# Kernel tuning notes

Measured on AMD Instinct MI355X. Metric: run time of the kernel, lower is better.

## Reference

```python
import jax, jax.numpy as jnp
import numpy as np

B, BARS, BEATS, FRAC = 64, 16, 4, 8
IN_F = 10 * 47 * 2  # 940
LIN_OUT = 100
BEAT_H = 16
BAR_H = 32


def _p(key, shape, scale=0.05):
    return jax.random.normal(key, shape, dtype=jnp.float32) * scale


def setup_inputs() -> dict:
    key = jax.random.key(0)
    ks = jax.random.split(key, 16)
    return {
        "channels": jax.random.normal(ks[0], (B, BARS, BEATS, FRAC, 10, 2, 47), dtype=jnp.float32),
        "lin_w": _p(ks[1], (LIN_OUT, IN_F)),
        "lin_b": _p(ks[2], (LIN_OUT,)),
        # beats LSTM (unidirectional), PyTorch gate order i,f,g,o
        "b_wih": _p(ks[3], (4 * BEAT_H, LIN_OUT)),
        "b_whh": _p(ks[4], (4 * BEAT_H, BEAT_H)),
        "b_bih": _p(ks[5], (4 * BEAT_H,)),
        "b_bhh": _p(ks[6], (4 * BEAT_H,)),
        # bars LSTM, bidirectional: forward (f_) and reverse (r_) directions
        "f_wih": _p(ks[7], (4 * BAR_H, BEAT_H)),
        "f_whh": _p(ks[8], (4 * BAR_H, BAR_H)),
        "f_bih": _p(ks[9], (4 * BAR_H,)),
        "f_bhh": _p(ks[10], (4 * BAR_H,)),
        "r_wih": _p(ks[11], (4 * BAR_H, BEAT_H)),
        "r_whh": _p(ks[12], (4 * BAR_H, BAR_H)),
        "r_bih": _p(ks[13], (4 * BAR_H,)),
        "r_bhh": _p(ks[14], (4 * BAR_H,)),
    }


def lstm(x, wih, whh, bih, bhh):
    """PyTorch-semantics LSTM, batch_first. x: [N, T, F] -> h_seq [N, T, H]."""
    N = x.shape[0]
    H = whh.shape[1]
    # precompute input contribution for all timesteps
    xg = jnp.einsum('ntf,gf->ntg', x, wih) + (bih + bhh)  # [N, T, 4H]

    def step(carry, xt):
        h, c = carry
        gates = xt + h @ whh.T  # [N, 4H]
        i, f, g, o = jnp.split(gates, 4, axis=-1)
        c = jax.nn.sigmoid(f) * c + jax.nn.sigmoid(i) * jnp.tanh(g)
        h = jax.nn.sigmoid(o) * jnp.tanh(c)
        return (h, c), h

    h0 = jnp.zeros((N, H), x.dtype)
    _, hs = jax.lax.scan(step, (h0, h0), jnp.swapaxes(xg, 0, 1))  # [T, N, H]
    return jnp.swapaxes(hs, 0, 1)


def bilstm(x, f_wih, f_whh, f_bih, f_bhh, r_wih, r_whh, r_bih, r_bhh):
    fwd = lstm(x, f_wih, f_whh, f_bih, f_bhh)
    bwd = jnp.flip(lstm(jnp.flip(x, axis=1), r_wih, r_whh, r_bih, r_bhh), axis=1)
    return jnp.concatenate([fwd, bwd], axis=-1)


def reference(channels, lin_w, lin_b,
              b_wih, b_whh, b_bih, b_bhh,
              f_wih, f_whh, f_bih, f_bhh,
              r_wih, r_whh, r_bih, r_bhh):
    # channels: [B, bars, beats, frac, 10, 2, 47]
    x = jnp.swapaxes(channels, -1, -2)  # [..., 10, 47, 2]
    x = x.reshape(*x.shape[:4], IN_F)   # squash dims 4..6 -> 940
    x = jax.nn.relu(x @ lin_w.T + lin_b)  # [B, bars, beats, frac, 100]

    # Distributed depth=2: fold (B, bars, beats) into batch, seq over frac
    xb = x.reshape(B * BARS * BEATS, FRAC, LIN_OUT)
    beats = lstm(xb, b_wih, b_whh, b_bih, b_bhh)
    beats = beats.reshape(B, BARS, BEATS, FRAC, BEAT_H)

    # last fraction hidden state, then Distributed depth=1 over beats axis
    xl = beats[:, :, :, -1].reshape(B * BARS, BEATS, BEAT_H)
    bars = bilstm(xl, f_wih, f_whh, f_bih, f_bhh, r_wih, r_whh, r_bih, r_bhh)
    bars = bars.reshape(B, BARS, BEATS, 2 * BAR_H)
    return beats, bars
```

## Files before the change

### kernel.cpp

```cpp
#include <hip/hip_runtime.h>
#include <hip/hip_bf16.h>

typedef float f32x4 __attribute__((ext_vector_type(4)));
typedef short bf16x8 __attribute__((ext_vector_type(8)));
typedef short bf16x4 __attribute__((ext_vector_type(4)));

#define MFMA16(a, b, c) __builtin_amdgcn_mfma_f32_16x16x32_bf16(a, b, c, 0, 0, 0)

constexpr int K1  = 940;
constexpr int KP2 = 1024;
constexpr int NP  = 112;
constexpr int OSL = 136;

__device__ __forceinline__ float sigf(float x) { return 1.f / (1.f + __expf(-x)); }
__device__ __forceinline__ float tanhfast(float x) { return 2.f / (1.f + __expf(-2.f * x)) - 1.f; }

__device__ __forceinline__ short f2b(float x) {
  __hip_bfloat16 b = __float2bfloat16(x);
  return *reinterpret_cast<short*>(&b);
}

__device__ __forceinline__ void lds_barrier() {
  asm volatile("s_waitcnt lgkmcnt(0)" ::: "memory");
  __builtin_amdgcn_s_barrier();
  __builtin_amdgcn_sched_barrier(0);
}

__global__ void prep_kernel(const float* __restrict__ lin_w,
                            const float* __restrict__ b_wih,
                            __hip_bfloat16* __restrict__ w2,
                            __hip_bfloat16* __restrict__ bw2) {
  int idx = blockIdx.x * 256 + threadIdx.x;
  if (idx < NP * KP2) {
    int n = idx >> 10, k = idx & 1023;
    float v = 0.f;
    if (n < 100 && k < K1) {
      int c10 = k / 94, rem = k - c10 * 94;
      int c2 = rem / 47, c47 = rem - c2 * 47;
      int f = c10 * 94 + c47 * 2 + c2;
      v = lin_w[n * K1 + f];
    }
    w2[idx] = __float2bfloat16(v);
  } else {
    int i2 = idx - NP * KP2;
    if (i2 < 64 * 128) {
      int g = i2 >> 7, k = i2 & 127;
      bw2[i2] = __float2bfloat16((k < 100) ? b_wih[g * 100 + k] : 0.f);
    }
  }
}

__global__ __launch_bounds__(256, 2)
void fused_encoder(const float* __restrict__ ch,
                   const __hip_bfloat16* __restrict__ w2,
                   const float* __restrict__ lin_b,
                   const __hip_bfloat16* __restrict__ bw2,
                   const float* __restrict__ bih,
                   const float* __restrict__ bhh,
                   const float* __restrict__ whh,
                   const float* __restrict__ fwih, const float* __restrict__ fwhh,
                   const float* __restrict__ fbih, const float* __restrict__ fbhh,
                   const float* __restrict__ rwih, const float* __restrict__ rwhh,
                   const float* __restrict__ rbih, const float* __restrict__ rbhh,
                   float* __restrict__ beats,
                   float* __restrict__ bars) {
  __shared__ __align__(16) char smem[45056];
  char* As = smem;
  char* Bw = smem + 16384;
  __hip_bfloat16* out_s = reinterpret_cast<__hip_bfloat16*>(smem);
  float*          xg_s  = reinterpret_cast<float*>(smem + 17408);
  float (*hlast)[16]    = reinterpret_cast<float(*)[16]>(smem + 34048);
  float (*hb)[32]       = reinterpret_cast<float(*)[32]>(smem + 34560);
  float (*gact)[128]    = reinterpret_cast<float(*)[128]>(smem + 34816);

  const int tid = threadIdx.x;
  const int w = tid >> 6, lane = tid & 63;
  const int l16 = lane & 15, bq = lane >> 4;

  float lb[7];
#pragma unroll
  for (int nt = 0; nt < 7; ++nt) {
    int col = nt * 16 + l16;
    lb[nt] = (col < 100) ? lin_b[col] : 0.f;
  }

  f32x4 acc[7] = {};
  float4 rA[8];
  bf16x8 bst[8];

  const float4 f40{0.f, 0.f, 0.f, 0.f};

  const int acolf = (lane & 31) * 4;
  const float* asrc = ch + (long)(blockIdx.x * 64 + w * 16 + (lane >> 5)) * K1 + acolf;
  auto ldA = [&](int c) {
    const float* p = asrc + c * 128;
    if (c < 7) {
#pragma unroll
      for (int j = 0; j < 8; ++j)
        rA[j] = *reinterpret_cast<const float4*>(p + (long)j * 2 * K1);
    } else {
      const bool ok = acolf < 44;
#pragma unroll
      for (int j = 0; j < 8; ++j)
        rA[j] = ok ? *reinterpret_cast<const float4*>(p + (long)j * 2 * K1) : f40;
    }
  };
  auto stA = [&]() {
#pragma unroll
    for (int j = 0; j < 8; ++j) {
      const int row = w * 16 + (lane >> 5) + 2 * j;
      const int byte = row * 256 + (((lane & 31) * 8) ^ ((row & 7) << 4));
      bf16x4 v = {f2b(rA[j].x), f2b(rA[j].y), f2b(rA[j].z), f2b(rA[j].w)};
      *reinterpret_cast<bf16x4*>(As + byte) = v;
    }
  };

  const int sn = tid >> 1;
  const int khb = (tid & 1) * 128;
  auto ldB = [&](int c) {
    if (sn < NP) {
      const __hip_bfloat16* src = w2 + sn * KP2 + c * 128 + (tid & 1) * 64;
#pragma unroll
      for (int j = 0; j < 8; ++j)
        bst[j] = *reinterpret_cast<const bf16x8*>(src + j * 8);
    }
  };
  auto stB = [&]() {
    if (sn < NP) {
      const int swz = (sn & 7) << 4;
#pragma unroll
      for (int j = 0; j < 8; ++j)
        *reinterpret_cast<bf16x8*>(Bw + sn * 256 + ((khb + j * 16) ^ swz)) = bst[j];
    }
  };

  ldA(0);
  ldB(0);

  const int fsw = (l16 & 7) << 4;
  const int abase = (w * 16 + l16) * 256;

#pragma unroll
  for (int c = 0; c < 8; ++c) {
    stA();
    stB();
    lds_barrier();
    if (c < 7) { ldA(c + 1); ldB(c + 1); }
#pragma unroll
    for (int ks = 0; ks < 4; ++ks) {
      const int ko = (ks * 64 + bq * 16);
      bf16x8 a = *reinterpret_cast<const bf16x8*>(As + abase + (ko ^ fsw));
#pragma unroll
      for (int nt = 0; nt < 7; ++nt) {
        bf16x8 b = *reinterpret_cast<const bf16x8*>(
            Bw + (nt * 16 + l16) * 256 + (ko ^ fsw));
        acc[nt] = MFMA16(a, b, acc[nt]);
      }
    }
    lds_barrier();
  }

#pragma unroll
  for (int nt = 0; nt < 7; ++nt) {
    const int col = nt * 16 + l16;
#pragma unroll
    for (int r = 0; r < 4; ++r) {
      float v = fmaxf(acc[nt][r] + lb[nt], 0.f);
      out_s[(w * 16 + bq * 4 + r) * OSL + col] = __float2bfloat16((col < 100) ? v : 0.f);
    }
  }
#pragma unroll
  for (int r = 0; r < 4; ++r)
    out_s[(w * 16 + bq * 4 + r) * OSL + 112 + l16] = __float2bfloat16(0.f);

  {
    bf16x8 av[4];
#pragma unroll
    for (int s = 0; s < 4; ++s)
      av[s] = *reinterpret_cast<const bf16x8*>(&out_s[(w * 16 + l16) * OSL + s * 32 + bq * 8]);
    f32x4 xacc[4] = {};
#pragma unroll
    for (int gt = 0; gt < 4; ++gt) {
#pragma unroll
      for (int s = 0; s < 4; ++s) {
        bf16x8 b = *reinterpret_cast<const bf16x8*>(&bw2[(gt * 16 + l16) * 128 + s * 32 + bq * 8]);
        xacc[gt] = MFMA16(av[s], b, xacc[gt]);
      }
    }
#pragma unroll
    for (int gt = 0; gt < 4; ++gt) {
      const int gate = gt * 16 + l16;
      const float bias = bih[gate] + bhh[gate];
#pragma unroll
      for (int r = 0; r < 4; ++r)
        xg_s[(w * 16 + bq * 4 + r) * 65 + gate] = xacc[gt][r] + bias;
    }
  }

  {
    const int cell = lane & 15;
    float wr[16];
#pragma unroll
    for (int u = 0; u < 16; ++u) wr[u] = whh[lane * 16 + u];
    float xv0[8], xv1[8];
#pragma unroll
    for (int t = 0; t < 8; ++t) {
      xv0[t] = xg_s[(w * 16 + t) * 65 + lane];
      xv1[t] = xg_s[(w * 16 + 8 + t) * 65 + lane];
    }
    float h0[16], h1[16];
#pragma unroll
    for (int u = 0; u < 16; ++u) { h0[u] = 0.f; h1[u] = 0.f; }
    float c0 = 0.f, c1 = 0.f;
    const long sg0 = (long)blockIdx.x * 8 + 2 * w;
    const long sg1 = sg0 + 1;
#pragma unroll
    for (int t = 0; t < 8; ++t) {
      float p0 = xv0[t], p1 = xv1[t];
#pragma unroll
      for (int u = 0; u < 16; ++u) { p0 += wr[u] * h0[u]; p1 += wr[u] * h1[u]; }
      const bool istanh = (lane >= 32 && lane < 48);
      float a0 = istanh ? tanhfast(p0) : sigf(p0);
      float a1 = istanh ? tanhfast(p1) : sigf(p1);
      float gi0 = __shfl(a0, cell),      gi1 = __shfl(a1, cell);
      float gf0 = __shfl(a0, cell + 16), gf1 = __shfl(a1, cell + 16);
      float gg0 = __shfl(a0, cell + 32), gg1 = __shfl(a1, cell + 32);
      float go0 = __shfl(a0, cell + 48), go1 = __shfl(a1, cell + 48);
      c0 = gf0 * c0 + gi0 * gg0;
      c1 = gf1 * c1 + gi1 * gg1;
      float hn0 = go0 * tanhfast(c0);
      float hn1 = go1 * tanhfast(c1);
#pragma unroll
      for (int u = 0; u < 16; ++u) { h0[u] = __shfl(hn0, u); h1[u] = __shfl(hn1, u); }
      if (lane < 16) {
        beats[sg0 * 128 + t * 16 + lane] = hn0;
        beats[sg1 * 128 + t * 16 + lane] = hn1;
        if (t == 7) {
          hlast[2 * w][lane]     = hn0;
          hlast[2 * w + 1][lane] = hn1;
        }
      }
    }
  }
  __syncthreads();

  {
    const int dir = tid >> 7, g = tid & 127;
    const float* wihp = dir ? rwih : fwih;
    const float* whhp = dir ? rwhh : fwhh;
    const float bias = dir ? (rbih[g] + rbhh[g]) : (fbih[g] + fbhh[g]);
    float wi[16], wh[32];
#pragma unroll
    for (int u = 0; u < 16; ++u) wi[u] = wihp[g * 16 + u];
#pragma unroll
    for (int u = 0; u < 32; ++u) wh[u] = whhp[g * 32 + u];
    for (int b2 = 0; b2 < 2; ++b2) {
      const int n = blockIdx.x * 2 + b2;
      float c = 0.f;
      if (g < 32) hb[dir][g] = 0.f;
      __syncthreads();
      for (int t = 0; t < 4; ++t) {
        const int tt = dir ? (3 - t) : t;
        float pre = bias;
#pragma unroll
        for (int u = 0; u < 16; ++u) pre += wi[u] * hlast[b2 * 4 + tt][u];
#pragma unroll
        for (int u = 0; u < 32; ++u) pre += wh[u] * hb[dir][u];
        gact[dir][g] = (g >= 64 && g < 96) ? tanhfast(pre) : sigf(pre);
        __syncthreads();
        if (g < 32) {
          c = gact[dir][32 + g] * c + gact[dir][g] * gact[dir][64 + g];
          float hn = gact[dir][96 + g] * tanhfast(c);
          hb[dir][g] = hn;
          bars[(n * 4 + tt) * 64 + dir * 32 + g] = hn;
        }
        __syncthreads();
      }
    }
  }
}

extern "C" void kernel_launch(void* const* d_in, const int* in_sizes, int n_in,
                              void* d_out, int out_size, void* d_ws, size_t ws_size,
                              hipStream_t stream) {
  const float* ch    = (const float*)d_in[0];
  const float* lin_w = (const float*)d_in[1];
  const float* lin_b = (const float*)d_in[2];
  const float* b_wih = (const float*)d_in[3];
  const float* b_whh = (const float*)d_in[4];
  const float* b_bih = (const float*)d_in[5];
  const float* b_bhh = (const float*)d_in[6];
  const float* f_wih = (const float*)d_in[7];
  const float* f_whh = (const float*)d_in[8];
  const float* f_bih = (const float*)d_in[9];
  const float* f_bhh = (const float*)d_in[10];
  const float* r_wih = (const float*)d_in[11];
  const float* r_whh = (const float*)d_in[12];
  const float* r_bih = (const float*)d_in[13];
  const float* r_bhh = (const float*)d_in[14];

  char* ws = (char*)d_ws;
  __hip_bfloat16* w2  = (__hip_bfloat16*)ws;
  __hip_bfloat16* bw2 = (__hip_bfloat16*)(ws + 229376);
  float*          out = (float*)d_out;

  prep_kernel<<<480, 256, 0, stream>>>(lin_w, b_wih, w2, bw2);
  fused_encoder<<<512, 256, 0, stream>>>(ch, w2, lin_b, bw2, b_bih, b_bhh,
                                         b_whh,
                                         f_wih, f_whh, f_bih, f_bhh,
                                         r_wih, r_whh, r_bih, r_bhh,
                                         out, out + 524288);
}
```

Measured before the change: 231.4 us.

## Split fused encoder into DMA-pipelined GEMM and separate LSTM kernel

The fused encoder is split into two kernels: a linear GEMM that writes bf16 activations to a workspace, and an LSTM kernel that reads them back. The GEMM now streams the weight matrix straight into LDS with global_load_lds. It uses double-buffered B tiles stored pre-swizzled in chunks by the prep kernel, and it overlaps the next chunk's loads with the current MFMAs. This aims to cut register staging and per-chunk barriers in the GEMM, and lets the LSTM kernel run with its own resource limits. In exchange it adds an extra launch and a global round trip for the intermediate activations.

Measured after the change: 234.1 us. No clear change (+1.2%).

```diff
diff --git a/kernel.cpp b/kernel.cpp
--- a/kernel.cpp
+++ b/kernel.cpp
@@ -8,9 +8,10 @@
 #define MFMA16(a, b, c) __builtin_amdgcn_mfma_f32_16x16x32_bf16(a, b, c, 0, 0, 0)
 
 constexpr int K1  = 940;
-constexpr int KP2 = 1024;
 constexpr int NP  = 112;
 constexpr int OSL = 136;
+constexpr int CHE = 14336;
+constexpr int CHB = 28672;
 
 __device__ __forceinline__ float sigf(float x) { return 1.f / (1.f + __expf(-x)); }
 __device__ __forceinline__ float tanhfast(float x) { return 2.f / (1.f + __expf(-2.f * x)) - 1.f; }
@@ -20,18 +21,18 @@
   return *reinterpret_cast<short*>(&b);
 }
 
-__device__ __forceinline__ void lds_barrier() {
-  asm volatile("s_waitcnt lgkmcnt(0)" ::: "memory");
-  __builtin_amdgcn_s_barrier();
-  __builtin_amdgcn_sched_barrier(0);
+__device__ __forceinline__ void gl_lds16(const void* g, void* l) {
+  __builtin_amdgcn_global_load_lds(
+      (const __attribute__((address_space(1))) unsigned int*)g,
+      (__attribute__((address_space(3))) unsigned int*)l, 16, 0, 0);
 }
 
 __global__ void prep_kernel(const float* __restrict__ lin_w,
                             const float* __restrict__ b_wih,
-                            __hip_bfloat16* __restrict__ w2,
+                            __hip_bfloat16* __restrict__ w2c,
                             __hip_bfloat16* __restrict__ bw2) {
   int idx = blockIdx.x * 256 + threadIdx.x;
-  if (idx < NP * KP2) {
+  if (idx < NP * 1024) {
     int n = idx >> 10, k = idx & 1023;
     float v = 0.f;
     if (n < 100 && k < K1) {
@@ -40,9 +41,10 @@
       int f = c10 * 94 + c47 * 2 + c2;
       v = lin_w[n * K1 + f];
     }
-    w2[idx] = __float2bfloat16(v);
+    int c = k >> 7, kk = k & 127;
+    w2c[c * CHE + n * 128 + (kk ^ ((n & 7) << 3))] = __float2bfloat16(v);
   } else {
-    int i2 = idx - NP * KP2;
+    int i2 = idx - NP * 1024;
     if (i2 < 64 * 128) {
       int g = i2 >> 7, k = i2 & 127;
       bw2[i2] = __float2bfloat16((k < 100) ? b_wih[g * 100 + k] : 0.f);
@@ -51,47 +53,23 @@
 }
 
 __global__ __launch_bounds__(256, 2)
-void fused_encoder(const float* __restrict__ ch,
-                   const __hip_bfloat16* __restrict__ w2,
-                   const float* __restrict__ lin_b,
-                   const __hip_bfloat16* __restrict__ bw2,
-                   const float* __restrict__ bih,
-                   const float* __restrict__ bhh,
-                   const float* __restrict__ whh,
-                   const float* __restrict__ fwih, const float* __restrict__ fwhh,
-                   const float* __restrict__ fbih, const float* __restrict__ fbhh,
-                   const float* __restrict__ rwih, const float* __restrict__ rwhh,
-                   const float* __restrict__ rbih, const float* __restrict__ rbhh,
-                   float* __restrict__ beats,
-                   float* __restrict__ bars) {
-  __shared__ __align__(16) char smem[45056];
+void linear_gemm(const float* __restrict__ ch,
+                 const __hip_bfloat16* __restrict__ w2c,
+                 const float* __restrict__ lin_b,
+                 __hip_bfloat16* __restrict__ out1) {
+  __shared__ __align__(16) char smem[73728];
   char* As = smem;
-  char* Bw = smem + 16384;
-  __hip_bfloat16* out_s = reinterpret_cast<__hip_bfloat16*>(smem);
-  float*          xg_s  = reinterpret_cast<float*>(smem + 17408);
-  float (*hlast)[16]    = reinterpret_cast<float(*)[16]>(smem + 34048);
-  float (*hb)[32]       = reinterpret_cast<float(*)[32]>(smem + 34560);
-  float (*gact)[128]    = reinterpret_cast<float(*)[128]>(smem + 34816);
+  char* Bs = smem + 16384;
 
   const int tid = threadIdx.x;
   const int w = tid >> 6, lane = tid & 63;
   const int l16 = lane & 15, bq = lane >> 4;
-
-  float lb[7];
-#pragma unroll
-  for (int nt = 0; nt < 7; ++nt) {
-    int col = nt * 16 + l16;
-    lb[nt] = (col < 100) ? lin_b[col] : 0.f;
-  }
-
-  f32x4 acc[7] = {};
+  const int row0 = blockIdx.x * 64 + w * 16;
+
   float4 rA[8];
-  bf16x8 bst[8];
-
   const float4 f40{0.f, 0.f, 0.f, 0.f};
-
   const int acolf = (lane & 31) * 4;
-  const float* asrc = ch + (long)(blockIdx.x * 64 + w * 16 + (lane >> 5)) * K1 + acolf;
+  const float* asrc = ch + (long)(row0 + (lane >> 5)) * K1 + acolf;
   auto ldA = [&](int c) {
     const float* p = asrc + c * 128;
     if (c < 7) {
@@ -115,63 +93,99 @@
     }
   };
 
-  const int sn = tid >> 1;
-  const int khb = (tid & 1) * 128;
-  auto ldB = [&](int c) {
-    if (sn < NP) {
-      const __hip_bfloat16* src = w2 + sn * KP2 + c * 128 + (tid & 1) * 64;
-#pragma unroll
-      for (int j = 0; j < 8; ++j)
-        bst[j] = *reinterpret_cast<const bf16x8*>(src + j * 8);
-    }
+  auto dmaB = [&](int c, int buf) {
+    const __hip_bfloat16* src = w2c + c * CHE + w * 3584 + lane * 8;
+    char* dst = Bs + buf * CHB + w * 7168;
+#pragma unroll
+    for (int j = 0; j < 7; ++j)
+      gl_lds16(src + j * 512, dst + j * 1024);
   };
-  auto stB = [&]() {
-    if (sn < NP) {
-      const int swz = (sn & 7) << 4;
-#pragma unroll
-      for (int j = 0; j < 8; ++j)
-        *reinterpret_cast<bf16x8*>(Bw + sn * 256 + ((khb + j * 16) ^ swz)) = bst[j];
-    }
-  };
 
   ldA(0);
-  ldB(0);
-
+  dmaB(0, 0);
+  stA();
+  asm volatile("s_waitcnt vmcnt(0) lgkmcnt(0)" ::: "memory");
+  __builtin_amdgcn_s_barrier();
+  __builtin_amdgcn_sched_barrier(0);
+
+  f32x4 acc[7] = {};
   const int fsw = (l16 & 7) << 4;
   const int abase = (w * 16 + l16) * 256;
 
 #pragma unroll
   for (int c = 0; c < 8; ++c) {
-    stA();
-    stB();
-    lds_barrier();
-    if (c < 7) { ldA(c + 1); ldB(c + 1); }
+    if (c < 7) {
+      ldA(c + 1);
+      dmaB(c + 1, (c + 1) & 1);
+    }
+    const char* Bp = Bs + (c & 1) * CHB;
 #pragma unroll
     for (int ks = 0; ks < 4; ++ks) {
-      const int ko = (ks * 64 + bq * 16);
-      bf16x8 a = *reinterpret_cast<const bf16x8*>(As + abase + (ko ^ fsw));
+      const int ko = (ks * 64 + bq * 16) ^ fsw;
+      bf16x8 a = *reinterpret_cast<const bf16x8*>(As + abase + ko);
 #pragma unroll
       for (int nt = 0; nt < 7; ++nt) {
-        bf16x8 b = *reinterpret_cast<const bf16x8*>(
-            Bw + (nt * 16 + l16) * 256 + (ko ^ fsw));
+        bf16x8 b = *reinterpret_cast<const bf16x8*>(Bp + (nt * 16 + l16) * 256 + ko);
         acc[nt] = MFMA16(a, b, acc[nt]);
       }
     }
-    lds_barrier();
+    asm volatile("s_waitcnt lgkmcnt(0)" ::: "memory");
+    if (c < 7) stA();
+    asm volatile("s_waitcnt vmcnt(0) lgkmcnt(0)" ::: "memory");
+    __builtin_amdgcn_s_barrier();
+    __builtin_amdgcn_sched_barrier(0);
   }
 
 #pragma unroll
   for (int nt = 0; nt < 7; ++nt) {
     const int col = nt * 16 + l16;
+    const float bias = (col < 100) ? lin_b[col] : 0.f;
 #pragma unroll
     for (int r = 0; r < 4; ++r) {
-      float v = fmaxf(acc[nt][r] + lb[nt], 0.f);
-      out_s[(w * 16 + bq * 4 + r) * OSL + col] = __float2bfloat16((col < 100) ? v : 0.f);
-    }
-  }
-#pragma unroll
-  for (int r = 0; r < 4; ++r)
-    out_s[(w * 16 + bq * 4 + r) * OSL + 112 + l16] = __float2bfloat16(0.f);
+      float v = (col < 100) ? fmaxf(acc[nt][r] + bias, 0.f) : 0.f;
+      out1[(long)(row0 + bq * 4 + r) * 112 + col] = __float2bfloat16(v);
+    }
+  }
+}
+
+__global__ __launch_bounds__(256)
+void lstm_kernel(const __hip_bfloat16* __restrict__ out1,
+                 const __hip_bfloat16* __restrict__ bw2,
+                 const float* __restrict__ bih,
+                 const float* __restrict__ bhh,
+                 const float* __restrict__ whh,
+                 const float* __restrict__ fwih, const float* __restrict__ fwhh,
+                 const float* __restrict__ fbih, const float* __restrict__ fbhh,
+                 const float* __restrict__ rwih, const float* __restrict__ rwhh,
+                 const float* __restrict__ rbih, const float* __restrict__ rbhh,
+                 float* __restrict__ beats,
+                 float* __restrict__ bars) {
+  __shared__ __align__(16) __hip_bfloat16 out_s[64 * OSL];
+  __shared__ float xg_s[64 * 65];
+  __shared__ float hlast[8][16];
+  __shared__ float hb[2][32];
+  __shared__ float gact[2][128];
+
+  const int tid = threadIdx.x;
+  const int w = tid >> 6, lane = tid & 63;
+  const int l16 = lane & 15, bq = lane >> 4;
+  const long rbase = (long)blockIdx.x * 64;
+
+#pragma unroll
+  for (int it = 0; it < 4; ++it) {
+    const int e = it * 256 + tid;
+    if (e < 896) {
+      const int row = e / 14, g = e - row * 14;
+      *reinterpret_cast<bf16x8*>(&out_s[row * OSL + g * 8]) =
+          *reinterpret_cast<const bf16x8*>(&out1[(rbase + row) * 112 + g * 8]);
+    }
+  }
+  if (tid < 128) {
+    const int row = tid >> 1, c0 = 112 + (tid & 1) * 8;
+    bf16x8 z = {0, 0, 0, 0, 0, 0, 0, 0};
+    *reinterpret_cast<bf16x8*>(&out_s[row * OSL + c0]) = z;
+  }
+  __syncthreads();
 
   {
     bf16x8 av[4];
@@ -300,14 +314,15 @@
   const float* r_bhh = (const float*)d_in[14];
 
   char* ws = (char*)d_ws;
-  __hip_bfloat16* w2  = (__hip_bfloat16*)ws;
-  __hip_bfloat16* bw2 = (__hip_bfloat16*)(ws + 229376);
-  float*          out = (float*)d_out;
-
-  prep_kernel<<<480, 256, 0, stream>>>(lin_w, b_wih, w2, bw2);
-  fused_encoder<<<512, 256, 0, stream>>>(ch, w2, lin_b, bw2, b_bih, b_bhh,
-                                         b_whh,
-                                         f_wih, f_whh, f_bih, f_bhh,
-                                         r_wih, r_whh, r_bih, r_bhh,
-                                         out, out + 524288);
-}
+  __hip_bfloat16* w2c  = (__hip_bfloat16*)ws;
+  __hip_bfloat16* bw2  = (__hip_bfloat16*)(ws + 229376);
+  __hip_bfloat16* out1 = (__hip_bfloat16*)(ws + 245760);
+  float*          out  = (float*)d_out;
+
+  prep_kernel<<<480, 256, 0, stream>>>(lin_w, b_wih, w2c, bw2);
+  linear_gemm<<<512, 256, 0, stream>>>(ch, w2c, lin_b, out1);
+  lstm_kernel<<<512, 256, 0, stream>>>(out1, bw2, b_bih, b_bhh, b_whh,
+                                       f_wih, f_whh, f_bih, f_bhh,
+                                       r_wih, r_whh, r_bih, r_bhh,
+                                       out, out + 524288);
+}
```
